# Kernel tuning notes

Measured on AMD Instinct MI355X. Metric: run time of the kernel, lower is better.

## Reference

```python
import jax, jax.numpy as jnp
import numpy as np

N_SAMPLES = 32768
SAMPLES_PER_FRAME = 256
N_FRAMES = N_SAMPLES // SAMPLES_PER_FRAME  # 128
SAMPLERATE = 22050
NYQUIST = SAMPLERATE // 2
MIN_FREQ = 40.0 / NYQUIST
MAX_FREQ = 4000.0 / NYQUIST
FREQ_SCALE = MAX_FREQ - MIN_FREQ
TWO_PI = 2.0 * np.pi


def lin_interp(x, out_size):
    """torch F.interpolate(mode='linear', align_corners=False) along last axis."""
    in_size = x.shape[-1]
    scale = in_size / out_size
    coords = (jnp.arange(out_size, dtype=x.dtype) + 0.5) * scale - 0.5
    coords = jnp.clip(coords, 0.0, in_size - 1)
    i0 = jnp.floor(coords).astype(jnp.int32)
    i1 = jnp.minimum(i0 + 1, in_size - 1)
    w = coords - i0.astype(x.dtype)
    return x[..., i0] * (1.0 - w) + x[..., i1] * w


def setup_inputs() -> dict:
    key = jax.random.key(0)
    k1, k2 = jax.random.split(key)
    f0 = jax.random.uniform(k1, (4, 16, 1), dtype=jnp.float32)  # normalized freq in [0,1)
    # resonance decay factors, realistic range near [0.75, 0.999)
    res = 0.75 + 0.249 * jax.random.uniform(k2, (4, 16, 32), dtype=jnp.float32)
    factors = jnp.arange(1, 33, dtype=jnp.float32)  # harmonic multipliers 1..32
    return {"f0": f0, "res": res, "factors": factors}


def reference(f0, res, factors):
    B, E, _ = f0.shape
    F_ = factors.shape[0]
    # map f0 in [0,1] to normalized frequency band
    f0 = MIN_FREQ + FREQ_SCALE * f0                      # (B, E, 1)
    freqs = f0 * factors[None, None, :]                  # (B, E, F)
    freqs = jnp.where(freqs >= 1.0, 0.0, freqs)          # zero out aliased harmonics
    # repeat per frame then upsample to sample rate
    freqs = jnp.broadcast_to(freqs[..., None], (B, E, F_, N_FRAMES))
    freqs = lin_interp(freqs, N_SAMPLES)                 # (B, E, F, N_SAMPLES)
    # exponential decay envelope: cumprod over frames via exp(cumsum(log))
    log_res = jnp.log(res + 1e-12)                       # (B, E, F)
    log_env = jnp.cumsum(
        jnp.broadcast_to(log_res[..., None], (B, E, F_, N_FRAMES)), axis=-1)
    env = jnp.exp(log_env)
    env = lin_interp(env, N_SAMPLES)                     # (B, E, F, N_SAMPLES)
    # integrate phase and oscillate
    phase = jnp.cumsum(freqs * TWO_PI, axis=-1)
    final = env * jnp.sin(phase)                         # (B, E, F, N_SAMPLES)
    return jnp.sum(final, axis=2)                        # (B, E, N_SAMPLES)
```

## Files before the change

### kernel.cpp

```cpp
#include <hip/hip_runtime.h>
#include <hip/hip_bf16.h>


#define NSAMP 32768
#define NFRM  128
#define NF    32
#define NPAIR 64
#define CHUNKS 16
#define CHUNK_SAMP (NSAMP / CHUNKS)
#define ITERS (CHUNK_SAMP / 256)

__device__ __forceinline__ float ldin(const void* p, int i, bool isbf) {
    if (isbf) {
        unsigned int w = ((unsigned int)((const unsigned short*)p)[i]) << 16;
        float f;
        __builtin_memcpy(&f, &w, 4);
        return f;
    }
    return ((const float*)p)[i];
}

extern "C" __global__ __launch_bounds__(256)
void reson_kernel(const void* __restrict__ f0p,
                  const void* __restrict__ resp,
                  const void* __restrict__ facp,
                  void* __restrict__ outp)
{
    const bool isbf = (((const unsigned int*)facp)[0] != 0x3F800000u);

    const int pair = blockIdx.x;
    const int tid  = threadIdx.x;

    __shared__ float P[NFRM * NF];
    __shared__ float FQ[NF];

    const float MINF = (float)(40.0 / 11025.0);
    const float FSC  = (float)(3960.0 / 11025.0);

    if (tid < NF) {
        float f0v = ldin(f0p, pair, isbf);
        float sf0 = MINF + FSC * f0v;
        float fac = ldin(facp, tid, isbf);
        float fr  = sf0 * fac;
        if (fr >= 1.0f) fr = 0.0f;
        FQ[tid] = fr;
    }
    for (int idx = tid; idx < NFRM * NF; idx += 256) {
        int t = idx >> 5;
        int f = idx & 31;
        float r = ldin(resp, pair * NF + f, isbf);
        P[idx] = exp2f(log2f(r) * (float)(t + 1));
    }
    __syncthreads();

    const int base = blockIdx.y * CHUNK_SAMP;

    for (int k = 0; k < ITERS; ++k) {
        const int n = base + k * 256 + tid;
        float c = (n + 0.5f) * (1.0f / 256.0f) - 0.5f;
        c = fminf(fmaxf(c, 0.0f), (float)(NFRM - 1));
        const int   i0 = (int)c;
        const int   i1 = min(i0 + 1, NFRM - 1);
        const float w  = c - (float)i0;
        const float* __restrict__ P0 = &P[i0 * NF];
        const float* __restrict__ P1 = &P[i1 * NF];

        const double np1 = (double)(n + 1);
        float acc = 0.0f;
        #pragma unroll
        for (int f = 0; f < NF; ++f) {
            float env = P0[f] * (1.0f - w) + P1[f] * w;
            double t = (double)FQ[f] * np1;
            t -= floor(t);
            float s = __builtin_amdgcn_sinf((float)t);
            acc = fmaf(env, s, acc);
        }

        const int o = pair * NSAMP + n;
        if (isbf) ((__hip_bfloat16*)outp)[o] = __float2bfloat16(acc);
        else      ((float*)outp)[o] = acc;
    }
}

extern "C" void kernel_launch(void* const* d_in, const int* in_sizes, int n_in,
                              void* d_out, int out_size, void* d_ws, size_t ws_size,
                              hipStream_t stream) {
    (void)in_sizes; (void)n_in; (void)out_size; (void)d_ws; (void)ws_size;
    dim3 grid(NPAIR, CHUNKS);
    dim3 block(256);
    reson_kernel<<<grid, block, 0, stream>>>(d_in[0], d_in[1], d_in[2], d_out);
}
```

Before: 79.40 us.

## Replace double-precision phase with 32-bit fixed-point and register envelope recurrence

Drops the shared-memory envelope table and the double-precision phase computation. Phase is now a 32-bit fixed-point product (Q*n wrapping mod 2^32), which removes the slow fp64 multiply and floor on each harmonic. The envelope is carried in registers as a running product with the decay factor across frame steps, which also removes the LDS reads and the sync. Precision risks come from truncating frequency to 32 bits and from accumulating the envelope by repeated multiplication instead of exp2 per frame, and register pressure rises.

```diff
diff --git a/kernel.cpp b/kernel.cpp
--- a/kernel.cpp
+++ b/kernel.cpp
@@ -7,8 +7,8 @@
 #define NF    32
 #define NPAIR 64
 #define CHUNKS 16
-#define CHUNK_SAMP (NSAMP / CHUNKS)
-#define ITERS (CHUNK_SAMP / 256)
+#define CHUNK (NSAMP / CHUNKS)
+#define KIT   (CHUNK / 256)
 
 __device__ __forceinline__ float ldin(const void* p, int i, bool isbf) {
     if (isbf) {
@@ -30,53 +30,70 @@
 
     const int pair = blockIdx.x;
     const int tid  = threadIdx.x;
-
-    __shared__ float P[NFRM * NF];
-    __shared__ float FQ[NF];
+    const int n0   = blockIdx.y * CHUNK + tid;
 
     const float MINF = (float)(40.0 / 11025.0);
     const float FSC  = (float)(3960.0 / 11025.0);
 
-    if (tid < NF) {
-        float f0v = ldin(f0p, pair, isbf);
-        float sf0 = MINF + FSC * f0v;
-        float fac = ldin(facp, tid, isbf);
+    const float f0v = ldin(f0p, pair, isbf);
+    const float sf0 = MINF + FSC * f0v;
+
+    const float c0raw = (n0 + 0.5f) * (1.0f / 256.0f) - 0.5f;
+    float c0 = fminf(fmaxf(c0raw, 0.0f), (float)(NFRM - 1));
+    const int   i0c = (int)c0;
+    const float w0  = c0 - (float)i0c;
+    const float c1  = c0raw + 1.0f;
+    const int   i01 = (int)c1;
+    const float w1  = c1 - (float)i01;
+    const bool  clampLow = (c0raw < 0.0f);
+
+    float A[NF], R[NF];
+    unsigned int Q[NF];
+    #pragma unroll
+    for (int f = 0; f < NF; ++f) {
+        const float r = ldin(resp, pair * NF + f, isbf);
+        R[f] = r;
+        float fac = ldin(facp, f, isbf);
         float fr  = sf0 * fac;
         if (fr >= 1.0f) fr = 0.0f;
-        FQ[tid] = fr;
+        Q[f] = (unsigned int)((double)fr * 4294967296.0);
+        A[f] = exp2f(log2f(r) * (float)(i0c + 1));
     }
-    for (int idx = tid; idx < NFRM * NF; idx += 256) {
-        int t = idx >> 5;
-        int f = idx & 31;
-        float r = ldin(resp, pair * NF + f, isbf);
-        P[idx] = exp2f(log2f(r) * (float)(t + 1));
-    }
-    __syncthreads();
 
-    const int base = blockIdx.y * CHUNK_SAMP;
+    const int obase = pair * NSAMP;
 
-    for (int k = 0; k < ITERS; ++k) {
-        const int n = base + k * 256 + tid;
-        float c = (n + 0.5f) * (1.0f / 256.0f) - 0.5f;
-        c = fminf(fmaxf(c, 0.0f), (float)(NFRM - 1));
-        const int   i0 = (int)c;
-        const int   i1 = min(i0 + 1, NFRM - 1);
-        const float w  = c - (float)i0;
-        const float* __restrict__ P0 = &P[i0 * NF];
-        const float* __restrict__ P1 = &P[i1 * NF];
-
-        const double np1 = (double)(n + 1);
+    {
+        unsigned int nn = (unsigned int)(n0 + 1);
         float acc = 0.0f;
         #pragma unroll
         for (int f = 0; f < NF; ++f) {
-            float env = P0[f] * (1.0f - w) + P1[f] * w;
-            double t = (double)FQ[f] * np1;
-            t -= floor(t);
-            float s = __builtin_amdgcn_sinf((float)t);
-            acc = fmaf(env, s, acc);
+            const float An  = A[f] * R[f];
+            const float env = fmaf(w0, An - A[f], A[f]);
+            const unsigned int ph = Q[f] * nn;
+            const float t = (float)ph * 0x1p-32f;
+            acc = fmaf(env, __builtin_amdgcn_sinf(t), acc);
+            A[f] = clampLow ? A[f] : An;
         }
+        const int o = obase + n0;
+        if (isbf) ((__hip_bfloat16*)outp)[o] = __float2bfloat16(acc);
+        else      ((float*)outp)[o] = acc;
+    }
 
-        const int o = pair * NSAMP + n;
+    for (int k = 1; k < KIT; ++k) {
+        const int n = n0 + k * 256;
+        const unsigned int nn = (unsigned int)(n + 1);
+        const float wk = (c0raw + (float)k > (float)(NFRM - 1)) ? 0.0f : w1;
+        float acc = 0.0f;
+        #pragma unroll
+        for (int f = 0; f < NF; ++f) {
+            const float An  = A[f] * R[f];
+            const float env = fmaf(wk, An - A[f], A[f]);
+            const unsigned int ph = Q[f] * nn;
+            const float t = (float)ph * 0x1p-32f;
+            acc = fmaf(env, __builtin_amdgcn_sinf(t), acc);
+            A[f] = An;
+        }
+        const int o = obase + n;
         if (isbf) ((__hip_bfloat16*)outp)[o] = __float2bfloat16(acc);
         else      ((float*)outp)[o] = acc;
     }
```

Result: slower. 83.57 us (+5.3%).
